# Kernel optimization log

Hardware: AMD Instinct MI355X
Metric: run time of the kernel (lower is better)

The kernel has to match this reference:

```python
import jax, jax.numpy as jnp
import numpy as np

B, T, D = 4, 4096, 2048
K = 1024
H, KVH, HD = 16, 4, 128
FF = 8192
EPS = 1e-6


def _rmsnorm(x, w):
    v = jnp.mean(x * x, axis=-1, keepdims=True)
    return x * jax.lax.rsqrt(v + EPS) * w


def _rotate_half(x):
    x1, x2 = jnp.split(x, 2, axis=-1)
    return jnp.concatenate([-x2, x1], axis=-1)


def setup_inputs() -> dict:
    key = jax.random.key(0)
    ks = jax.random.split(key, 16)
    hidden_states = jax.random.normal(ks[0], (B, T, D), dtype=jnp.float32)
    # unique sorted indices per sequence (top-k selection without duplicates)
    scores = jax.random.uniform(ks[1], (B, T))
    topk_indices = jnp.sort(jax.lax.top_k(scores, K)[1], axis=-1).astype(jnp.int64)
    gating_scores = jax.random.uniform(ks[2], (B, K), dtype=jnp.float32)
    # rotary embeddings over the full sequence [B, T, HD]
    inv = 1.0 / (10000.0 ** (jnp.arange(0, HD, 2, dtype=jnp.float32) / HD))
    ang = jnp.arange(T, dtype=jnp.float32)[:, None] * inv[None, :]  # [T, HD/2]
    emb = jnp.concatenate([ang, ang], axis=-1)
    cos = jnp.broadcast_to(jnp.cos(emb)[None], (B, T, HD)).astype(jnp.float32)
    sin = jnp.broadcast_to(jnp.sin(emb)[None], (B, T, HD)).astype(jnp.float32)
    s = 0.02
    params = dict(
        Wq=jax.random.normal(ks[3], (D, H * HD)) * s,
        bq=jnp.zeros((H * HD,)),
        Wk=jax.random.normal(ks[4], (D, KVH * HD)) * s,
        bk=jnp.zeros((KVH * HD,)),
        Wv=jax.random.normal(ks[5], (D, KVH * HD)) * s,
        bv=jnp.zeros((KVH * HD,)),
        Wo=jax.random.normal(ks[6], (H * HD, D)) * s,
        w_gate=jax.random.normal(ks[7], (D, FF)) * s,
        w_up=jax.random.normal(ks[8], (D, FF)) * s,
        w_down=jax.random.normal(ks[9], (FF, D)) * s,
        ln1_w=jnp.ones((D,)),
        ln2_w=jnp.ones((D,)),
    )
    return dict(hidden_states=hidden_states, topk_indices=topk_indices,
                gating_scores=gating_scores, cos=cos, sin=sin, **params)


def _decoder_layer(x, cos_s, sin_s, Wq, bq, Wk, bk, Wv, bv, Wo,
                   w_gate, w_up, w_down, ln1_w, ln2_w):
    # x: [B, K, D]; cos_s/sin_s: [B, K, HD]
    res = x
    h = _rmsnorm(x, ln1_w)
    q = (h @ Wq + bq).reshape(B, K, H, HD)
    k = (h @ Wk + bk).reshape(B, K, KVH, HD)
    v = (h @ Wv + bv).reshape(B, K, KVH, HD)
    c = cos_s[:, :, None, :]
    s = sin_s[:, :, None, :]
    q = q * c + _rotate_half(q) * s
    k = k * c + _rotate_half(k) * s
    # GQA: repeat kv heads
    k = jnp.repeat(k, H // KVH, axis=2)
    v = jnp.repeat(v, H // KVH, axis=2)
    scores = jnp.einsum('bqhd,bkhd->bhqk', q, k) / np.sqrt(HD)
    causal = jnp.tril(jnp.ones((K, K), dtype=bool))
    scores = jnp.where(causal[None, None], scores, jnp.finfo(scores.dtype).min)
    attn = jax.nn.softmax(scores, axis=-1)
    out = jnp.einsum('bhqk,bkhd->bqhd', attn, v).reshape(B, K, H * HD)
    x = res + out @ Wo
    # MLP (SwiGLU)
    res = x
    h = _rmsnorm(x, ln2_w)
    x = res + (jax.nn.silu(h @ w_gate) * (h @ w_up)) @ w_down
    return x


def reference(hidden_states, topk_indices, gating_scores, cos, sin,
              Wq, bq, Wk, bk, Wv, bv, Wo, w_gate, w_up, w_down, ln1_w, ln2_w):
    idx = topk_indices[:, :, None]  # [B, K, 1]
    selected = jnp.take_along_axis(hidden_states, idx, axis=1)  # [B, K, D]
    cos_s = jnp.take_along_axis(cos, idx, axis=1)
    sin_s = jnp.take_along_axis(sin, idx, axis=1)
    processed = _decoder_layer(selected, cos_s, sin_s, Wq, bq, Wk, bk, Wv, bv,
                               Wo, w_gate, w_up, w_down, ln1_w, ln2_w)
    # soft gating: selected + gate * (processed - selected)
    updated = selected + (processed - selected) * gating_scores[:, :, None]
    b_idx = jnp.arange(B)[:, None]
    final = hidden_states.at[b_idx, topk_indices].set(updated)
    return final
```

## Files before the change

### kernel.cpp

```cpp
#include <hip/hip_runtime.h>
#include <stdint.h>

typedef __bf16 bf16;
typedef __attribute__((ext_vector_type(8))) __bf16 bf16x8;
typedef __attribute__((ext_vector_type(4))) float f32x4;

namespace {

constexpr int cB = 4, cT = 4096, cD = 2048, cK = 1024, cH = 16, cKVH = 4, cHD = 128, cFF = 8192;
constexpr int cM = cB * cK;
constexpr int QKVW = cH * cHD + 2 * cKVH * cHD;

__device__ __forceinline__ void load_lds16(const void* g, void* l) {
  __builtin_amdgcn_global_load_lds((const __attribute__((address_space(1))) void*)g,
                                   (__attribute__((address_space(3))) void*)l, 16, 0, 0);
}

template <int N>
__device__ __forceinline__ void waitcnt_vm() {
  if constexpr (N == 0) asm volatile("s_waitcnt vmcnt(0)" ::: "memory");
  else if constexpr (N == 3) asm volatile("s_waitcnt vmcnt(3)" ::: "memory");
  else if constexpr (N == 4) asm volatile("s_waitcnt vmcnt(4)" ::: "memory");
  else if constexpr (N == 6) asm volatile("s_waitcnt vmcnt(6)" ::: "memory");
  else if constexpr (N == 8) asm volatile("s_waitcnt vmcnt(8)" ::: "memory");
  else if constexpr (N == 9) asm volatile("s_waitcnt vmcnt(9)" ::: "memory");
  else if constexpr (N == 12) asm volatile("s_waitcnt vmcnt(12)" ::: "memory");
  else static_assert(N == 0, "unsupported vmcnt literal");
}

template <int OP>
__device__ __forceinline__ float blk_reduce(float v) {
  __shared__ float sm[5];
  const int tid = threadIdx.x, lane = tid & 63, wid = tid >> 6;
#pragma unroll
  for (int o = 32; o; o >>= 1) {
    float o2 = __shfl_down(v, o, 64);
    v = OP ? fmaxf(v, o2) : v + o2;
  }
  if (lane == 0) sm[wid] = v;
  __syncthreads();
  if (tid == 0) {
    float r = sm[0];
#pragma unroll
    for (int i = 1; i < 4; ++i) r = OP ? fmaxf(r, sm[i]) : r + sm[i];
    sm[4] = r;
  }
  __syncthreads();
  float r = sm[4];
  __syncthreads();
  return r;
}

template <int BN, int WM, int WN, int RING, int UNROLL, class Epi>
__global__ __launch_bounds__(512, 2)
void gemm256(const bf16* __restrict__ A, int lda,
             const bf16* __restrict__ Bm, int ldb,
             int Kd, int GM, Epi epi) {
  constexpr int BM = 256;
  constexpr int FM = BM / WM / 16;
  constexpr int FN = BN / WN / 16;
  constexpr int ACALLS = 2;
  constexpr int BCALLS = BN / 128;
  constexpr int L = ACALLS + BCALLS;
  constexpr int D = RING - 1;
  constexpr int SLOTA = BM * 64;
  constexpr int SLOTB = BN * 64;
  constexpr int SLOT = SLOTA + SLOTB;
  __shared__ __align__(16) char lds[RING * SLOT];

  const int tid = threadIdx.x;
  const int lane = tid & 63;
  const int wid = tid >> 6;
  const int l15 = lane & 15, lq = lane >> 4;
  const int wr = wid / WN, wc = wid % WN;

  const int nwg = gridDim.x;
  const int xcd = blockIdx.x & 7, loc = blockIdx.x >> 3;
  const int wg = xcd * (nwg >> 3) + loc;
  const int GN = nwg / GM;
  const int per = 8 * GN;
  const int g = wg / per, r = wg % per;
  const int bm = g * 8 + (r & 7);
  const int bn = r >> 3;

  const bf16* Abase = A + (int64_t)bm * BM * lda;
  const bf16* Bbase = Bm + (int64_t)bn * BN * ldb;

  const bf16* srcA[ACALLS];
  int dstA[ACALLS];
#pragma unroll
  for (int c2 = 0; c2 < ACALLS; ++c2) {
    const int chunk = c2 * 512 + tid;
    const int row = chunk >> 2, pc = chunk & 3;
    const int lc = pc ^ ((row >> 1) & 3);
    srcA[c2] = Abase + (int64_t)row * lda + lc * 8;
    dstA[c2] = chunk * 16;
  }
  const bf16* srcB[BCALLS];
  int dstB[BCALLS];
#pragma unroll
  for (int c2 = 0; c2 < BCALLS; ++c2) {
    const int chunk = c2 * 512 + tid;
    const int row = chunk >> 2, pc = chunk & 3;
    const int lc = pc ^ ((row >> 1) & 3);
    srcB[c2] = Bbase + (int64_t)row * ldb + lc * 8;
    dstB[c2] = chunk * 16;
  }

  int offA[FM], offB[FN];
#pragma unroll
  for (int m = 0; m < FM; ++m) {
    const int row = wr * (BM / WM) + m * 16 + l15;
    offA[m] = row * 64 + (lq ^ ((row >> 1) & 3)) * 16;
  }
#pragma unroll
  for (int n = 0; n < FN; ++n) {
    const int row = wc * (BN / WN) + n * 16 + l15;
    offB[n] = SLOTA + row * 64 + (lq ^ ((row >> 1) & 3)) * 16;
  }

  const int KT = Kd >> 5;
  auto stage = [&](int t) {
    char* sb = lds + (size_t)(t % RING) * SLOT;
#pragma unroll
    for (int c2 = 0; c2 < ACALLS; ++c2)
      load_lds16(srcA[c2] + t * 32, sb + dstA[c2]);
#pragma unroll
    for (int c2 = 0; c2 < BCALLS; ++c2)
      load_lds16(srcB[c2] + t * 32, sb + SLOTA + dstB[c2]);
  };
  auto compute = [&](int t, f32x4 (&acc)[FM][FN]) {
    const char* sb = lds + (size_t)(t % RING) * SLOT;
    bf16x8 av[FM], bv[FN];
#pragma unroll
    for (int m = 0; m < FM; ++m) av[m] = *(const bf16x8*)(sb + offA[m]);
#pragma unroll
    for (int n = 0; n < FN; ++n) bv[n] = *(const bf16x8*)(sb + offB[n]);
    __builtin_amdgcn_s_setprio(1);
#pragma unroll
    for (int m = 0; m < FM; ++m)
#pragma unroll
      for (int n = 0; n < FN; ++n)
        acc[m][n] = __builtin_amdgcn_mfma_f32_16x16x32_bf16(av[m], bv[n], acc[m][n], 0, 0, 0);
    __builtin_amdgcn_s_setprio(0);
  };

  f32x4 acc[FM][FN] = {};

  if constexpr (UNROLL == 1) {
#pragma unroll
    for (int i = 0; i < D; ++i) stage(i);
    waitcnt_vm<(D - 1) * L>();
    __builtin_amdgcn_s_barrier();
    __builtin_amdgcn_sched_barrier(0);
    for (int t = 0; t < KT - D; ++t) {
      stage(t + D);
      compute(t, acc);
      waitcnt_vm<(D - 1) * L>();
      __builtin_amdgcn_s_barrier();
      __builtin_amdgcn_sched_barrier(0);
    }
    waitcnt_vm<0>();
    __builtin_amdgcn_s_barrier();
    for (int t = KT - D; t < KT; ++t) compute(t, acc);
  } else {
    static_assert(RING == 5 && UNROLL == 2, "pair mode is RING=5");
#pragma unroll
    for (int i = 0; i < 3; ++i) stage(i);
    waitcnt_vm<L>();
    __builtin_amdgcn_s_barrier();
    __builtin_amdgcn_sched_barrier(0);
    int t = 0;
    for (; t <= KT - 6; t += 2) {
      stage(t + 3);
      stage(t + 4);
      compute(t, acc);
      compute(t + 1, acc);
      waitcnt_vm<L>();
      __builtin_amdgcn_s_barrier();
      __builtin_amdgcn_sched_barrier(0);
    }
    stage(KT - 1);
    waitcnt_vm<0>();
    __builtin_amdgcn_s_barrier();
    compute(KT - 4, acc);
    compute(KT - 3, acc);
    compute(KT - 2, acc);
    compute(KT - 1, acc);
  }

#pragma unroll
  for (int m = 0; m < FM; ++m) {
    const int r0 = bm * BM + wr * (BM / WM) + m * 16 + lq * 4;
#pragma unroll
    for (int n = 0; n < FN; ++n) {
      const int c1 = bn * BN + wc * (BN / WN) + n * 16 + l15;
#pragma unroll
      for (int j = 0; j < 4; ++j) epi(r0 + j, c1, acc[m][n][j]);
    }
  }
}

__global__ __launch_bounds__(512, 2)
void gemm_gateup(const bf16* __restrict__ A, const bf16* __restrict__ Bg,
                 const bf16* __restrict__ Bu, bf16* __restrict__ act) {
  constexpr int BM = 256, BN = 128, WM = 4, WN = 2;
  constexpr int FM = 4, FN = 4;
  constexpr int RING = 5, L = 4;
  constexpr int SLOTA = BM * 64, SLOTB = BN * 64;
  constexpr int SLOT = SLOTA + 2 * SLOTB;
  __shared__ __align__(16) char lds[RING * SLOT];

  const int tid = threadIdx.x;
  const int lane = tid & 63;
  const int wid = tid >> 6;
  const int l15 = lane & 15, lq = lane >> 4;
  const int wr = wid / WN, wc = wid % WN;

  const int nwg = gridDim.x;
  const int xcd = blockIdx.x & 7, loc = blockIdx.x >> 3;
  const int wg = xcd * (nwg >> 3) + loc;
  const int GM = 16, GN = nwg / GM;
  const int per = 8 * GN;
  const int g = wg / per, r = wg % per;
  const int bm = g * 8 + (r & 7);
  const int bn = r >> 3;

  const bf16* Abase = A + (int64_t)bm * BM * cD;
  const bf16* Gbase = Bg + (int64_t)bn * BN * cD;
  const bf16* Ubase = Bu + (int64_t)bn * BN * cD;

  const bf16* srcA[2];
  int dstA[2];
#pragma unroll
  for (int c2 = 0; c2 < 2; ++c2) {
    const int chunk = c2 * 512 + tid;
    const int row = chunk >> 2, pc = chunk & 3;
    const int lc = pc ^ ((row >> 1) & 3);
    srcA[c2] = Abase + (int64_t)row * cD + lc * 8;
    dstA[c2] = chunk * 16;
  }
  const int brow = tid >> 2, bpc = tid & 3;
  const int blc = bpc ^ ((brow >> 1) & 3);
  const bf16* srcG = Gbase + (int64_t)brow * cD + blc * 8;
  const bf16* srcU = Ubase + (int64_t)brow * cD + blc * 8;
  const int dstBo = tid * 16;

  int offA[FM], offB[FN];
#pragma unroll
  for (int m = 0; m < FM; ++m) {
    const int row = wr * 64 + m * 16 + l15;
    offA[m] = row * 64 + (lq ^ ((row >> 1) & 3)) * 16;
  }
#pragma unroll
  for (int n = 0; n < FN; ++n) {
    const int row = wc * 64 + n * 16 + l15;
    offB[n] = row * 64 + (lq ^ ((row >> 1) & 3)) * 16;
  }

  const int KT = cD >> 5;
  auto stage = [&](int t) {
    char* sb = lds + (size_t)(t % RING) * SLOT;
#pragma unroll
    for (int c2 = 0; c2 < 2; ++c2) load_lds16(srcA[c2] + t * 32, sb + dstA[c2]);
    load_lds16(srcG + t * 32, sb + SLOTA + dstBo);
    load_lds16(srcU + t * 32, sb + SLOTA + SLOTB + dstBo);
  };

  f32x4 accg[FM][FN] = {}, accu[FM][FN] = {};

  auto compute = [&](int t) {
    const char* sb = lds + (size_t)(t % RING) * SLOT;
    bf16x8 av[FM], gv[FN], uv[FN];
#pragma unroll
    for (int m = 0; m < FM; ++m) av[m] = *(const bf16x8*)(sb + offA[m]);
#pragma unroll
    for (int n = 0; n < FN; ++n) gv[n] = *(const bf16x8*)(sb + SLOTA + offB[n]);
#pragma unroll
    for (int n = 0; n < FN; ++n) uv[n] = *(const bf16x8*)(sb + SLOTA + SLOTB + offB[n]);
    __builtin_amdgcn_s_setprio(1);
#pragma unroll
    for (int m = 0; m < FM; ++m)
#pragma unroll
      for (int n = 0; n < FN; ++n) {
        accg[m][n] = __builtin_amdgcn_mfma_f32_16x16x32_bf16(av[m], gv[n], accg[m][n], 0, 0, 0);
        accu[m][n] = __builtin_amdgcn_mfma_f32_16x16x32_bf16(av[m], uv[n], accu[m][n], 0, 0, 0);
      }
    __builtin_amdgcn_s_setprio(0);
  };

#pragma unroll
  for (int i = 0; i < 3; ++i) stage(i);
  waitcnt_vm<L>();
  __builtin_amdgcn_s_barrier();
  __builtin_amdgcn_sched_barrier(0);
  int t = 0;
  for (; t <= KT - 6; t += 2) {
    stage(t + 3);
    stage(t + 4);
    compute(t);
    compute(t + 1);
    waitcnt_vm<L>();
    __builtin_amdgcn_s_barrier();
    __builtin_amdgcn_sched_barrier(0);
  }
  stage(KT - 1);
  waitcnt_vm<0>();
  __builtin_amdgcn_s_barrier();
  compute(KT - 4);
  compute(KT - 3);
  compute(KT - 2);
  compute(KT - 1);

#pragma unroll
  for (int m = 0; m < FM; ++m) {
    const int r0 = bm * BM + wr * 64 + m * 16 + lq * 4;
#pragma unroll
    for (int n = 0; n < FN; ++n) {
      const int c1 = bn * BN + wc * 64 + n * 16 + l15;
#pragma unroll
      for (int j = 0; j < 4; ++j) {
        float gvv = accg[m][n][j];
        float s = gvv / (1.f + __expf(-gvv));
        act[(int64_t)(r0 + j) * cFF + c1] = (bf16)(s * accu[m][n][j]);
      }
    }
  }
}

struct EpiQKV {
  bf16* out; const float* bias;
  __device__ void operator()(int r, int c, float v) const {
    out[(int64_t)r * QKVW + c] = (bf16)(v + bias[c]);
  }
};
struct EpiOProj {
  float* x; const float* hidden; const int* topk;
  __device__ void operator()(int r, int c, float v) const {
    int b = r >> 10;
    int t = topk[r];
    x[(int64_t)r * cD + c] = v + hidden[((int64_t)b * cT + t) * cD + c];
  }
};
struct EpiDown {
  float* out; const float* x; const float* hidden; const int* topk; const float* gating;
  __device__ void operator()(int r, int c, float v) const {
    int b = r >> 10;
    int t = topk[r];
    float x2 = v + x[(int64_t)r * cD + c];
    int64_t ho = ((int64_t)b * cT + t) * cD + c;
    float sel = hidden[ho];
    out[ho] = sel + (x2 - sel) * gating[r];
  }
};

__global__ __launch_bounds__(256, 2) void flash_attn(const bf16* __restrict__ qkv,
                                                     const bf16* __restrict__ vt,
                                                     bf16* __restrict__ outb) {
  constexpr int QB = 64, KVB = 128;
  __shared__ __align__(16) char lds[81920];
  char* sK = lds;
  char* sP = lds + 32768;
  char* sV = lds + 49152;

  const int qt = blockIdx.x, h = blockIdx.y, b = blockIdx.z;
  const int kvh = h >> 2;
  const int qlo = qt * QB;
  const int tid = threadIdx.x, lane = tid & 63, wid = tid >> 6;
  const int l15 = lane & 15, lq = lane >> 4;
  const int wid16 = wid * 16;

  const bf16* qbase = qkv + (int64_t)(b * cK + qlo) * QKVW + h * cHD;
  const bf16* kbase = qkv + (int64_t)(b * cK) * QKVW + cH * cHD + kvh * cHD;
  const bf16* vtbase = vt + (int64_t)(b * cKVH + kvh) * cHD * cK;

#pragma unroll
  for (int c2 = 0; c2 < 4; ++c2) {
    int chunk = c2 * 256 + tid;
    int row = chunk >> 4, c16 = chunk & 15;
    load_lds16(qbase + (int64_t)row * QKVW + (c16 ^ (row & 15)) * 8, sK + chunk * 16);
  }
  __syncthreads();
  bf16x8 qf[4];
  {
    const int row = wid16 + l15;
#pragma unroll
    for (int kt = 0; kt < 4; ++kt)
      qf[kt] = *(const bf16x8*)(sK + row * 256 + (((kt * 4 + lq) ^ (row & 15)) * 16));
  }
  __syncthreads();

  f32x4 oacc[8] = {};
  float m_run[4], l_run[4];
#pragma unroll
  for (int j = 0; j < 4; ++j) { m_run[j] = -3.0e38f; l_run[j] = 0.f; }

  const int jmax = (qlo + QB - 1) >> 7;
  const float sl2e = 0.08838834764831845f * 1.44269504088896f;

  for (int jj = 0; jj <= jmax; ++jj) {
#pragma unroll
    for (int c2 = 0; c2 < 8; ++c2) {
      int chunk = c2 * 256 + tid;
      int row = chunk >> 4, c16 = chunk & 15;
      int cs = (c16 ^ (row & 15)) * 8;
      load_lds16(kbase + (int64_t)(jj * KVB + row) * QKVW + cs, sK + chunk * 16);
      load_lds16(vtbase + (int64_t)row * cK + jj * KVB + cs, sV + chunk * 16);
    }
    __syncthreads();

    f32x4 sacc[8] = {};
#pragma unroll
    for (int kt = 0; kt < 4; ++kt) {
      bf16x8 bv[8];
#pragma unroll
      for (int n = 0; n < 8; ++n) {
        int rk = n * 16 + l15;
        bv[n] = *(const bf16x8*)(sK + rk * 256 + (((kt * 4 + lq) ^ (rk & 15)) * 16));
      }
#pragma unroll
      for (int n = 0; n < 8; ++n)
        sacc[n] = __builtin_amdgcn_mfma_f32_16x16x32_bf16(qf[kt], bv[n], sacc[n], 0, 0, 0);
    }

    if (jj == jmax) {
#pragma unroll
      for (int n = 0; n < 8; ++n)
#pragma unroll
        for (int j = 0; j < 4; ++j) {
          int qrow = qlo + wid16 + lq * 4 + j;
          int kcol = jj * KVB + n * 16 + l15;
          if (kcol > qrow) sacc[n][j] = -3.0e38f;
        }
    }

#pragma unroll
    for (int j = 0; j < 4; ++j) {
      float mx = sacc[0][j];
#pragma unroll
      for (int n = 1; n < 8; ++n) mx = fmaxf(mx, sacc[n][j]);
#pragma unroll
      for (int off = 1; off < 16; off <<= 1) mx = fmaxf(mx, __shfl_xor(mx, off, 64));
      float mnew = fmaxf(m_run[j], mx);
      float corr = exp2f((m_run[j] - mnew) * sl2e);
      m_run[j] = mnew;
      float ps = 0.f;
#pragma unroll
      for (int n = 0; n < 8; ++n) {
        float p = exp2f((sacc[n][j] - mnew) * sl2e);
        sacc[n][j] = p;
        ps += p;
      }
#pragma unroll
      for (int off = 1; off < 16; off <<= 1) ps += __shfl_xor(ps, off, 64);
      l_run[j] = l_run[j] * corr + ps;
#pragma unroll
      for (int n = 0; n < 8; ++n) oacc[n][j] *= corr;
    }

#pragma unroll
    for (int n = 0; n < 8; ++n)
#pragma unroll
      for (int j = 0; j < 4; ++j) {
        int row = wid16 + lq * 4 + j;
        int col = n * 16 + l15;
        int c16 = (col >> 3) ^ (row & 15);
        *(bf16*)(sP + row * 256 + c16 * 16 + (col & 7) * 2) = (bf16)sacc[n][j];
      }
    __syncthreads();

#pragma unroll
    for (int kt = 0; kt < 4; ++kt) {
      const int prow = wid16 + l15;
      bf16x8 av = *(const bf16x8*)(sP + prow * 256 + (((kt * 4 + lq) ^ (prow & 15)) * 16));
      bf16x8 bv[8];
#pragma unroll
      for (int n = 0; n < 8; ++n) {
        int rd = n * 16 + l15;
        bv[n] = *(const bf16x8*)(sV + rd * 256 + (((kt * 4 + lq) ^ (rd & 15)) * 16));
      }
#pragma unroll
      for (int n = 0; n < 8; ++n)
        oacc[n] = __builtin_amdgcn_mfma_f32_16x16x32_bf16(av, bv[n], oacc[n], 0, 0, 0);
    }
    __syncthreads();
  }

#pragma unroll
  for (int j = 0; j < 4; ++j) {
    int row = qlo + wid16 + lq * 4 + j;
    float inv = 1.f / l_run[j];
#pragma unroll
    for (int n = 0; n < 8; ++n) {
      int col = h * cHD + n * 16 + l15;
      outb[((int64_t)b * cK + row) * cD + col] = (bf16)(oacc[n][j] * inv);
    }
  }
}

__global__ void copy_skip(const float4* __restrict__ s, float4* __restrict__ d,
                          const unsigned char* __restrict__ flags, int64_t n) {
  int64_t i = (int64_t)blockIdx.x * blockDim.x + threadIdx.x;
  const int64_t st = (int64_t)gridDim.x * blockDim.x;
  for (; i < n; i += st) {
    int row = (int)(i >> 9);
    if (!flags[row]) d[i] = s[i];
  }
}

__global__ void build_flags(const int* __restrict__ topk, unsigned char* __restrict__ flags) {
  int r = blockIdx.x * 256 + threadIdx.x;
  if (r < cM) flags[(r >> 10) * cT + topk[r]] = 1;
}

__global__ void wconv(const float* __restrict__ src, bf16* __restrict__ dst,
                      int R, int C, int coff, int ldd) {
  __shared__ float t[32][33];
  const int c0 = blockIdx.x * 32, r0 = blockIdx.y * 32;
  for (int rr = threadIdx.y; rr < 32; rr += 8)
    t[rr][threadIdx.x] = src[(int64_t)(r0 + rr) * C + c0 + threadIdx.x];
  __syncthreads();
  for (int rr = threadIdx.y; rr < 32; rr += 8)
    dst[(int64_t)(c0 + rr + coff) * ldd + r0 + threadIdx.x] = (bf16)t[threadIdx.x][rr];
}

__global__ void biascat(const float* __restrict__ bq, const float* __restrict__ bk,
                        const float* __restrict__ bv, float* __restrict__ o) {
  int i = blockIdx.x * 256 + threadIdx.x;
  if (i < QKVW) o[i] = (i < 2048) ? bq[i] : (i < 2560 ? bk[i - 2048] : bv[i - 2560]);
}

__global__ void rmsnorm_rows(const float* __restrict__ base, const int* __restrict__ topk,
                             const float* __restrict__ w, bf16* __restrict__ out) {
  const int r = blockIdx.x;
  const float* src;
  if (topk) {
    int t = topk[r];
    src = base + ((int64_t)(r >> 10) * cT + t) * cD;
  } else {
    src = base + (int64_t)r * cD;
  }
  const int tid = threadIdx.x;
  const float4* s4 = (const float4*)src;
  float4 a = s4[tid * 2], b = s4[tid * 2 + 1];
  float ss = a.x * a.x + a.y * a.y + a.z * a.z + a.w * a.w +
             b.x * b.x + b.y * b.y + b.z * b.z + b.w * b.w;
  float tot = blk_reduce<0>(ss);
  float sc = rsqrtf(tot * (1.f / cD) + 1e-6f);
  bf16* o = out + (int64_t)r * cD;
  const int d0 = tid * 8;
  o[d0 + 0] = (bf16)(a.x * sc * w[d0 + 0]);
  o[d0 + 1] = (bf16)(a.y * sc * w[d0 + 1]);
  o[d0 + 2] = (bf16)(a.z * sc * w[d0 + 2]);
  o[d0 + 3] = (bf16)(a.w * sc * w[d0 + 3]);
  o[d0 + 4] = (bf16)(b.x * sc * w[d0 + 4]);
  o[d0 + 5] = (bf16)(b.y * sc * w[d0 + 5]);
  o[d0 + 6] = (bf16)(b.z * sc * w[d0 + 6]);
  o[d0 + 7] = (bf16)(b.w * sc * w[d0 + 7]);
}

__global__ void rope_kernel(bf16* __restrict__ qkv, const float* __restrict__ cosb,
                            const float* __restrict__ sinb, const int* __restrict__ topk) {
  const int r = blockIdx.x;
  const int b = r >> 10;
  const int t = topk[r];
  const float* cr = cosb + ((int64_t)b * cT + t) * cHD;
  const float* sr = sinb + ((int64_t)b * cT + t) * cHD;
  bf16* rowq = qkv + (int64_t)r * QKVW;
  for (int p = threadIdx.x; p < (cH + cKVH) * 64; p += 256) {
    int hh = p >> 6, d = p & 63;
    bf16* base = (hh < cH) ? (rowq + hh * cHD) : (rowq + cH * cHD + (hh - cH) * cHD);
    float x1 = (float)base[d], x2 = (float)base[d + 64];
    float c1 = cr[d], s1 = sr[d], c2 = cr[d + 64], s2 = sr[d + 64];
    base[d] = (bf16)(x1 * c1 - x2 * s1);
    base[d + 64] = (bf16)(x2 * c2 + x1 * s2);
  }
}

__global__ void vtrans(const bf16* __restrict__ qkv, bf16* __restrict__ Vt) {
  __shared__ bf16 t[32][33];
  const int bz = blockIdx.z, b = bz >> 2, kv = bz & 3;
  const int k0 = blockIdx.x * 32, d0 = blockIdx.y * 32;
  for (int rr = threadIdx.y; rr < 32; rr += 8)
    t[rr][threadIdx.x] =
        qkv[(int64_t)(b * cK + k0 + rr) * QKVW + cH * cHD + cKVH * cHD + kv * cHD + d0 + threadIdx.x];
  __syncthreads();
  for (int rr = threadIdx.y; rr < 32; rr += 8)
    Vt[((int64_t)(b * cKVH + kv) * cHD + d0 + rr) * cK + k0 + threadIdx.x] = t[threadIdx.x][rr];
}

}

extern "C" void kernel_launch(void* const* d_in, const int* in_sizes, int n_in,
                              void* d_out, int out_size, void* d_ws, size_t ws_size,
                              hipStream_t stream) {
  const float* hidden = (const float*)d_in[0];
  const int* topk = (const int*)d_in[1];
  const float* gating = (const float*)d_in[2];
  const float* cosb = (const float*)d_in[3];
  const float* sinb = (const float*)d_in[4];
  const float* Wq = (const float*)d_in[5];
  const float* bq = (const float*)d_in[6];
  const float* Wk = (const float*)d_in[7];
  const float* bk = (const float*)d_in[8];
  const float* Wv = (const float*)d_in[9];
  const float* bv = (const float*)d_in[10];
  const float* Wo = (const float*)d_in[11];
  const float* wg = (const float*)d_in[12];
  const float* wu = (const float*)d_in[13];
  const float* wd = (const float*)d_in[14];
  const float* ln1 = (const float*)d_in[15];
  const float* ln2 = (const float*)d_in[16];
  float* out = (float*)d_out;
  (void)in_sizes; (void)n_in; (void)out_size; (void)ws_size;

  char* ws = (char*)d_ws;
  size_t off = 0;
  auto alloc = [&](size_t bytes) {
    char* p = ws + off;
    off += (bytes + 255) & ~(size_t)255;
    return p;
  };
  bf16* wt_qkv = (bf16*)alloc((size_t)QKVW * cD * 2);
  bf16* wt_o = (bf16*)alloc((size_t)cD * cD * 2);
  bf16* wt_g = (bf16*)alloc((size_t)cFF * cD * 2);
  bf16* wt_u = (bf16*)alloc((size_t)cFF * cD * 2);
  bf16* wt_d = (bf16*)alloc((size_t)cD * cFF * 2);
  float* bias_cat = (float*)alloc((size_t)QKVW * 4);
  bf16* hbuf = (bf16*)alloc((size_t)cM * cD * 2);
  bf16* qkv = (bf16*)alloc((size_t)cM * QKVW * 2);
  bf16* vt = (bf16*)alloc((size_t)cB * cKVH * cHD * cK * 2);
  bf16* attnout = (bf16*)alloc((size_t)cM * cD * 2);
  float* xbuf = (float*)alloc((size_t)cM * cD * 4);
  bf16* actbuf = (bf16*)alloc((size_t)cM * cFF * 2);
  unsigned char* flags = (unsigned char*)alloc((size_t)cB * cT);

  hipMemsetAsync(flags, 0, (size_t)cB * cT, stream);
  build_flags<<<cM / 256, 256, 0, stream>>>(topk, flags);
  copy_skip<<<2048, 256, 0, stream>>>((const float4*)hidden, (float4*)out, flags,
                                      (int64_t)cB * cT * cD / 4);

  const dim3 tb(32, 8);
  wconv<<<dim3(cD / 32, cD / 32), tb, 0, stream>>>(Wq, wt_qkv, cD, cD, 0, cD);
  wconv<<<dim3(512 / 32, cD / 32), tb, 0, stream>>>(Wk, wt_qkv, cD, 512, 2048, cD);
  wconv<<<dim3(512 / 32, cD / 32), tb, 0, stream>>>(Wv, wt_qkv, cD, 512, 2560, cD);
  wconv<<<dim3(cD / 32, cD / 32), tb, 0, stream>>>(Wo, wt_o, cD, cD, 0, cD);
  wconv<<<dim3(cFF / 32, cD / 32), tb, 0, stream>>>(wg, wt_g, cD, cFF, 0, cD);
  wconv<<<dim3(cFF / 32, cD / 32), tb, 0, stream>>>(wu, wt_u, cD, cFF, 0, cD);
  wconv<<<dim3(cD / 32, cFF / 32), tb, 0, stream>>>(wd, wt_d, cFF, cD, 0, cFF);
  biascat<<<(QKVW + 255) / 256, 256, 0, stream>>>(bq, bk, bv, bias_cat);

  rmsnorm_rows<<<cM, 256, 0, stream>>>(hidden, topk, ln1, hbuf);
  gemm256<256, 2, 4, 5, 2, EpiQKV><<<16 * (QKVW / 256), 512, 0, stream>>>(
      hbuf, cD, wt_qkv, cD, cD, 16, EpiQKV{qkv, bias_cat});
  rope_kernel<<<cM, 256, 0, stream>>>(qkv, cosb, sinb, topk);
  vtrans<<<dim3(cK / 32, cHD / 32, cB * cKVH), tb, 0, stream>>>(qkv, vt);

  flash_attn<<<dim3(cK / 64, cH, cB), 256, 0, stream>>>(qkv, vt, attnout);

  gemm256<128, 4, 2, 5, 2, EpiOProj><<<16 * (cD / 128), 512, 0, stream>>>(
      attnout, cD, wt_o, cD, cD, 16, EpiOProj{xbuf, hidden, topk});
  rmsnorm_rows<<<cM, 256, 0, stream>>>(xbuf, nullptr, ln2, hbuf);
  gemm_gateup<<<16 * (cFF / 128), 512, 0, stream>>>(hbuf, wt_g, wt_u, actbuf);
  gemm256<128, 4, 2, 5, 2, EpiDown><<<16 * (cD / 128), 512, 0, stream>>>(
      actbuf, cFF, wt_d, cFF, cFF, 16, EpiDown{out, xbuf, hidden, topk, gating});
}
```

Before: 869.5 us.

## Load gate/up weight fragments directly to registers, stage only A in LDS

Restructures the fused gate/up GEMM so each wave reads its B fragments (gate and up weights) straight from global memory into registers, while only the A tile goes through a 4-slot LDS ring with a depth-2 prefetch. The wave layout changes to 2x4, with each wave covering 128 rows by 32 columns. The aim is to cut LDS footprint and LDS read traffic for B and raise reuse of A fragments across more MFMAs. In exchange, B loads come uncoalesced per lane straight from global memory every k-step with little latency hiding. There is also a barrier on every iteration instead of every two.

```diff
diff --git a/kernel.cpp b/kernel.cpp
--- a/kernel.cpp
+++ b/kernel.cpp
@@ -204,31 +204,26 @@
 __global__ __launch_bounds__(512, 2)
 void gemm_gateup(const bf16* __restrict__ A, const bf16* __restrict__ Bg,
                  const bf16* __restrict__ Bu, bf16* __restrict__ act) {
-  constexpr int BM = 256, BN = 128, WM = 4, WN = 2;
-  constexpr int FM = 4, FN = 4;
-  constexpr int RING = 5, L = 4;
-  constexpr int SLOTA = BM * 64, SLOTB = BN * 64;
-  constexpr int SLOT = SLOTA + 2 * SLOTB;
-  __shared__ __align__(16) char lds[RING * SLOT];
+  constexpr int BM = 256;
+  constexpr int SLOTA = BM * 64;
+  __shared__ __align__(16) char lds[4 * SLOTA];
 
   const int tid = threadIdx.x;
   const int lane = tid & 63;
   const int wid = tid >> 6;
   const int l15 = lane & 15, lq = lane >> 4;
-  const int wr = wid / WN, wc = wid % WN;
+  const int wr = wid >> 2, wc = wid & 3;
 
   const int nwg = gridDim.x;
   const int xcd = blockIdx.x & 7, loc = blockIdx.x >> 3;
   const int wg = xcd * (nwg >> 3) + loc;
   const int GM = 16, GN = nwg / GM;
   const int per = 8 * GN;
-  const int g = wg / per, r = wg % per;
-  const int bm = g * 8 + (r & 7);
+  const int gg = wg / per, r = wg % per;
+  const int bm = gg * 8 + (r & 7);
   const int bn = r >> 3;
 
   const bf16* Abase = A + (int64_t)bm * BM * cD;
-  const bf16* Gbase = Bg + (int64_t)bn * BN * cD;
-  const bf16* Ubase = Bu + (int64_t)bn * BN * cD;
 
   const bf16* srcA[2];
   int dstA[2];
@@ -240,88 +235,65 @@
     srcA[c2] = Abase + (int64_t)row * cD + lc * 8;
     dstA[c2] = chunk * 16;
   }
-  const int brow = tid >> 2, bpc = tid & 3;
-  const int blc = bpc ^ ((brow >> 1) & 3);
-  const bf16* srcG = Gbase + (int64_t)brow * cD + blc * 8;
-  const bf16* srcU = Ubase + (int64_t)brow * cD + blc * 8;
-  const int dstBo = tid * 16;
-
-  int offA[FM], offB[FN];
-#pragma unroll
-  for (int m = 0; m < FM; ++m) {
-    const int row = wr * 64 + m * 16 + l15;
+
+  const int rk0 = bn * 128 + wc * 32 + l15;
+  const bf16* pG = Bg + (int64_t)rk0 * cD + lq * 8;
+  const bf16* pU = Bu + (int64_t)rk0 * cD + lq * 8;
+
+  int offA[8];
+#pragma unroll
+  for (int m = 0; m < 8; ++m) {
+    const int row = wr * 128 + m * 16 + l15;
     offA[m] = row * 64 + (lq ^ ((row >> 1) & 3)) * 16;
   }
-#pragma unroll
-  for (int n = 0; n < FN; ++n) {
-    const int row = wc * 64 + n * 16 + l15;
-    offB[n] = row * 64 + (lq ^ ((row >> 1) & 3)) * 16;
-  }
 
   const int KT = cD >> 5;
-  auto stage = [&](int t) {
-    char* sb = lds + (size_t)(t % RING) * SLOT;
-#pragma unroll
-    for (int c2 = 0; c2 < 2; ++c2) load_lds16(srcA[c2] + t * 32, sb + dstA[c2]);
-    load_lds16(srcG + t * 32, sb + SLOTA + dstBo);
-    load_lds16(srcU + t * 32, sb + SLOTA + SLOTB + dstBo);
+  auto stageA = [&](int t) {
+    char* sb = lds + (size_t)(t & 3) * SLOTA;
+    load_lds16(srcA[0] + t * 32, sb + dstA[0]);
+    load_lds16(srcA[1] + t * 32, sb + dstA[1]);
   };
 
-  f32x4 accg[FM][FN] = {}, accu[FM][FN] = {};
-
-  auto compute = [&](int t) {
-    const char* sb = lds + (size_t)(t % RING) * SLOT;
-    bf16x8 av[FM], gv[FN], uv[FN];
-#pragma unroll
-    for (int m = 0; m < FM; ++m) av[m] = *(const bf16x8*)(sb + offA[m]);
-#pragma unroll
-    for (int n = 0; n < FN; ++n) gv[n] = *(const bf16x8*)(sb + SLOTA + offB[n]);
-#pragma unroll
-    for (int n = 0; n < FN; ++n) uv[n] = *(const bf16x8*)(sb + SLOTA + SLOTB + offB[n]);
+  f32x4 accg[8][2] = {}, accu[8][2] = {};
+
+  stageA(0);
+  stageA(1);
+  for (int t = 0; t < KT; ++t) {
+    bf16x8 gfr0 = *(const bf16x8*)(pG + t * 32);
+    bf16x8 gfr1 = *(const bf16x8*)(pG + t * 32 + 16 * cD);
+    bf16x8 ufr0 = *(const bf16x8*)(pU + t * 32);
+    bf16x8 ufr1 = *(const bf16x8*)(pU + t * 32 + 16 * cD);
+    asm volatile("" ::: "memory");
+    if (t + 2 < KT) stageA(t + 2);
+    asm volatile("" ::: "memory");
+    waitcnt_vm<8>();
+    __builtin_amdgcn_s_barrier();
+    asm volatile("" ::: "memory");
+    const char* sb = lds + (size_t)(t & 3) * SLOTA;
+    bf16x8 av[8];
+#pragma unroll
+    for (int m = 0; m < 8; ++m) av[m] = *(const bf16x8*)(sb + offA[m]);
     __builtin_amdgcn_s_setprio(1);
 #pragma unroll
-    for (int m = 0; m < FM; ++m)
-#pragma unroll
-      for (int n = 0; n < FN; ++n) {
-        accg[m][n] = __builtin_amdgcn_mfma_f32_16x16x32_bf16(av[m], gv[n], accg[m][n], 0, 0, 0);
-        accu[m][n] = __builtin_amdgcn_mfma_f32_16x16x32_bf16(av[m], uv[n], accu[m][n], 0, 0, 0);
-      }
+    for (int m = 0; m < 8; ++m) {
+      accg[m][0] = __builtin_amdgcn_mfma_f32_16x16x32_bf16(av[m], gfr0, accg[m][0], 0, 0, 0);
+      accg[m][1] = __builtin_amdgcn_mfma_f32_16x16x32_bf16(av[m], gfr1, accg[m][1], 0, 0, 0);
+      accu[m][0] = __builtin_amdgcn_mfma_f32_16x16x32_bf16(av[m], ufr0, accu[m][0], 0, 0, 0);
+      accu[m][1] = __builtin_amdgcn_mfma_f32_16x16x32_bf16(av[m], ufr1, accu[m][1], 0, 0, 0);
+    }
     __builtin_amdgcn_s_setprio(0);
-  };
-
-#pragma unroll
-  for (int i = 0; i < 3; ++i) stage(i);
-  waitcnt_vm<L>();
-  __builtin_amdgcn_s_barrier();
-  __builtin_amdgcn_sched_barrier(0);
-  int t = 0;
-  for (; t <= KT - 6; t += 2) {
-    stage(t + 3);
-    stage(t + 4);
-    compute(t);
-    compute(t + 1);
-    waitcnt_vm<L>();
-    __builtin_amdgcn_s_barrier();
-    __builtin_amdgcn_sched_barrier(0);
-  }
-  stage(KT - 1);
-  waitcnt_vm<0>();
-  __builtin_amdgcn_s_barrier();
-  compute(KT - 4);
-  compute(KT - 3);
-  compute(KT - 2);
-  compute(KT - 1);
-
-#pragma unroll
-  for (int m = 0; m < FM; ++m) {
-    const int r0 = bm * BM + wr * 64 + m * 16 + lq * 4;
-#pragma unroll
-    for (int n = 0; n < FN; ++n) {
-      const int c1 = bn * BN + wc * 64 + n * 16 + l15;
+  }
+
+#pragma unroll
+  for (int m = 0; m < 8; ++m) {
+    const int r0 = bm * BM + wr * 128 + m * 16 + lq * 4;
+#pragma unroll
+    for (int n = 0; n < 2; ++n) {
+      const int c1 = bn * 128 + wc * 32 + n * 16 + l15;
 #pragma unroll
       for (int j = 0; j < 4; ++j) {
-        float gvv = accg[m][n][j];
-        float s = gvv / (1.f + __expf(-gvv));
+        float gv = accg[m][n][j];
+        float s = gv / (1.f + __expf(-gv));
         act[(int64_t)(r0 + j) * cFF + c1] = (bf16)(s * accu[m][n][j]);
       }
     }
```

Measured after the change: 922.8 us. 6.1% more time.
